# Kernel tuning notes

Hardware: AMD Instinct MI355X
Metric: run time of the kernel (lower is better)

## Reference

```python
import jax, jax.numpy as jnp
import numpy as np

B, S, E = 4, 2048, 1024
H = 16
D = E // H  # head dim = 64
ROPE_BASE = 10000.0


def _rope(t):
    # t: [B, H, S, D]; rotate-half RoPE (YaRN with scale=1 reduces to this)
    half = D // 2
    inv_freq = 1.0 / (ROPE_BASE ** (jnp.arange(0, half, dtype=jnp.float32) / half))
    pos = jnp.arange(t.shape[2], dtype=jnp.float32)
    ang = pos[:, None] * inv_freq[None, :]          # [S, D/2]
    cos, sin = jnp.cos(ang), jnp.sin(ang)
    t1, t2 = t[..., :half], t[..., half:]
    return jnp.concatenate([t1 * cos - t2 * sin, t1 * sin + t2 * cos], axis=-1)


def setup_inputs() -> dict:
    key = jax.random.key(0)
    ks = jax.random.split(key, 6)
    sc = 1.0 / np.sqrt(E)
    return {
        "x": jax.random.normal(ks[0], (B, S, E), jnp.float32),
        "Wq": jax.random.normal(ks[1], (E, E), jnp.float32) * sc,
        "Wk": jax.random.normal(ks[2], (E, E), jnp.float32) * sc,
        "Wv": jax.random.normal(ks[3], (E, E), jnp.float32) * sc,
        "Wp": jax.random.normal(ks[4], (E, E), jnp.float32) * sc,
        "bp": jnp.zeros((E,), jnp.float32),
    }


def reference(x, Wq, Wk, Wv, Wp, bp):
    seq = x.shape[1]
    def heads(W):
        # project then split heads -> [B, H, S, D]
        return (x @ W.T).reshape(B, seq, H, D).transpose(0, 2, 1, 3)
    q = _rope(heads(Wq))
    k = _rope(heads(Wk))
    v = heads(Wv)
    score = jnp.einsum("bhqd,bhkd->bhqk", q, k) * (D ** -0.5)
    mask = jnp.tril(jnp.ones((seq, seq), dtype=bool))
    score = jnp.where(mask[None, None], score, -jnp.inf)
    attn = jax.nn.softmax(score, axis=-1)
    out = jnp.einsum("bhqk,bhkd->bhqd", attn, v)
    out = out.transpose(0, 2, 1, 3).reshape(B, seq, E)
    return out @ Wp.T + bp  # dropout is identity at inference
```

## Files before the change

### kernel.cpp

```cpp
#include <hip/hip_runtime.h>
#include <hip/hip_bf16.h>

typedef __hip_bfloat16 bf16;
typedef __attribute__((ext_vector_type(8))) short bf16x8;
typedef __attribute__((ext_vector_type(4))) short bf16x4;
typedef __attribute__((ext_vector_type(4))) float f32x4;

static constexpr int B_ = 4, S_ = 2048, E_ = 1024, H_ = 16, D_ = 64;
static constexpr int M_ = B_ * S_;
static constexpr int NQKV = 3 * E_;

__device__ __forceinline__ void gload_lds16(const void* g, void* l) {
  __builtin_amdgcn_global_load_lds(
      (const __attribute__((address_space(1))) unsigned int*)g,
      (__attribute__((address_space(3))) unsigned int*)l, 16, 0, 0);
}

__device__ __forceinline__ void cast8(const float* __restrict__ src,
                                      bf16* __restrict__ dst, int t) {
  float4 a = ((const float4*)src)[2 * t];
  float4 b = ((const float4*)src)[2 * t + 1];
  union { bf16x8 v; bf16 e[8]; } u;
  u.e[0] = __float2bfloat16(a.x); u.e[1] = __float2bfloat16(a.y);
  u.e[2] = __float2bfloat16(a.z); u.e[3] = __float2bfloat16(a.w);
  u.e[4] = __float2bfloat16(b.x); u.e[5] = __float2bfloat16(b.y);
  u.e[6] = __float2bfloat16(b.z); u.e[7] = __float2bfloat16(b.w);
  ((bf16x8*)dst)[t] = u.v;
}

__global__ void prep_kernel(const float* __restrict__ x, const float* __restrict__ Wq,
                            const float* __restrict__ Wk, const float* __restrict__ Wv,
                            const float* __restrict__ Wp,
                            bf16* __restrict__ x_bf, bf16* __restrict__ w_bf,
                            float2* __restrict__ qtab, float2* __restrict__ ktab) {
  int bid = blockIdx.x;
  if (bid < 4096) {
    cast8(x, x_bf, bid * 256 + threadIdx.x);
  } else if (bid < 6144) {
    int wi = (bid - 4096) >> 9;
    const float* src = wi == 0 ? Wq : wi == 1 ? Wk : wi == 2 ? Wv : Wp;
    cast8(src, w_bf + (size_t)wi * E_ * E_, ((bid - 4096) & 511) * 256 + threadIdx.x);
  } else {
    int tt = (bid - 6144) * 256 + threadIdx.x;
    int i = tt & 31, s = tt >> 5;
    float inv_freq = powf(10000.0f, -(float)i / 32.0f);
    float ang = (float)s * inv_freq;
    float c = cosf(ang), sn = sinf(ang);
    const float qsc = 0.18033688011112043f;
    qtab[tt] = make_float2(c * qsc, sn * qsc);
    ktab[tt] = make_float2(c, sn);
  }
}

template <int OUTMODE>
__launch_bounds__(256)
__global__ void gemm_bt_kernel(const bf16* __restrict__ A, int lda,
                               const bf16* __restrict__ Bw, int ldb,
                               void* __restrict__ Cv, int ldc,
                               const float* __restrict__ bias,
                               int K, int ntiles_n,
                               const float2* __restrict__ qtab,
                               const float2* __restrict__ ktab,
                               bf16* __restrict__ qh,
                               bf16* __restrict__ khsw,
                               bf16* __restrict__ vtsw) {
  __shared__ bf16 Asm[128 * 64];
  __shared__ bf16 Bsm[128 * 64];
  int t = threadIdx.x;
  int lane = t & 63, w = t >> 6;
  int wr = w >> 1, wc = w & 1;
  int l15 = lane & 15, l4 = lane >> 4;
  int n0 = (blockIdx.x % ntiles_n) * 128;
  int m0 = (blockIdx.x / ntiles_n) * 128;

  f32x4 acc[4][4];
#pragma unroll
  for (int i = 0; i < 4; i++)
#pragma unroll
    for (int j = 0; j < 4; j++) acc[i][j] = (f32x4){0.f, 0.f, 0.f, 0.f};

  for (int k0 = 0; k0 < K; k0 += 64) {
#pragma unroll
    for (int p = 0; p < 4; p++) {
      int c = p * 256 + t;
      int row = c >> 3, kg = c & 7;
      int kgs = kg ^ (row & 7);
      const bf16* ga = A + (size_t)(m0 + row) * lda + k0 + kgs * 8;
      gload_lds16(ga, &Asm[(p * 256 + w * 64) * 8]);
      const bf16* gb = Bw + (size_t)(n0 + row) * ldb + k0 + kgs * 8;
      gload_lds16(gb, &Bsm[(p * 256 + w * 64) * 8]);
    }
    __syncthreads();
#pragma unroll
    for (int kk = 0; kk < 2; kk++) {
      bf16x8 am[4], bn[4];
#pragma unroll
      for (int i = 0; i < 4; i++) {
        int ra = wr * 64 + i * 16 + l15;
        am[i] = *(const bf16x8*)&Asm[ra * 64 + ((kk * 32 + l4 * 8) ^ ((ra & 7) * 8))];
        int rb = wc * 64 + i * 16 + l15;
        bn[i] = *(const bf16x8*)&Bsm[rb * 64 + ((kk * 32 + l4 * 8) ^ ((rb & 7) * 8))];
      }
#pragma unroll
      for (int i = 0; i < 4; i++)
#pragma unroll
        for (int j = 0; j < 4; j++)
          acc[i][j] = __builtin_amdgcn_mfma_f32_16x16x32_bf16(am[i], bn[j], acc[i][j], 0, 0, 0);
    }
    __syncthreads();
  }

  if (OUTMODE == 1) {
#pragma unroll
    for (int i = 0; i < 4; i++)
#pragma unroll
      for (int j = 0; j < 4; j++)
#pragma unroll
        for (int r = 0; r < 4; r++) {
          int m = m0 + wr * 64 + i * 16 + l4 * 4 + r;
          int n = n0 + wc * 64 + j * 16 + l15;
          ((float*)Cv)[(size_t)m * ldc + n] = acc[i][j][r] + bias[n];
        }
  } else {
    int btype = n0 >> 10;
    int h = ((n0 & 1023) >> 6) + wc;
    if (btype < 2) {
      const float2* tab = (btype == 0) ? qtab : ktab;
#pragma unroll
      for (int i = 0; i < 4; i++) {
        int mbase = m0 + wr * 64 + i * 16 + l4 * 4;
#pragma unroll
        for (int r = 0; r < 4; r++) {
          int m = mbase + r;
          int s = m & 2047, b = m >> 11;
#pragma unroll
          for (int j = 0; j < 2; j++) {
            int d1 = j * 16 + l15;
            float2 cs = tab[s * 32 + d1];
            float t1 = acc[i][j][r], t2 = acc[i][j + 2][r];
            bf16 o1 = __float2bfloat16(t1 * cs.x - t2 * cs.y);
            bf16 o2 = __float2bfloat16(t1 * cs.y + t2 * cs.x);
            if (btype == 0) {
              bf16* dst = qh + ((size_t)(b * H_ + h) * S_ + s) * D_;
              dst[d1] = o1;
              dst[d1 + 32] = o2;
            } else {
              int row = s & 63, kt = s >> 6, sz = (row & 7) * 8;
              bf16* dst = khsw + (((size_t)(b * H_ + h) * 32 + kt) * 64 + row) * 64;
              dst[d1 ^ sz] = o1;
              dst[(d1 + 32) ^ sz] = o2;
            }
          }
        }
      }
    } else {
#pragma unroll
      for (int i = 0; i < 4; i++) {
        int mbase = m0 + wr * 64 + i * 16 + l4 * 4;
        int c0 = mbase & 63, kt = (mbase >> 6) & 31, b = mbase >> 11;
#pragma unroll
        for (int j = 0; j < 4; j++) {
          int d = j * 16 + l15;
          union { bf16x4 v; short e[4]; } pk;
#pragma unroll
          for (int r = 0; r < 4; r++) {
            bf16 tv = __float2bfloat16(acc[i][j][r]);
            pk.e[r] = *(short*)&tv;
          }
          *(bf16x4*)&vtsw[(((size_t)(b * H_ + h) * 32 + kt) * 64 + d) * 64 +
                          (c0 ^ ((d & 7) * 8))] = pk.v;
        }
      }
    }
  }
}

__launch_bounds__(256, 3)
__global__ void attn_kernel(const bf16* __restrict__ qh, const bf16* __restrict__ khsw,
                            const bf16* __restrict__ vtsw, bf16* __restrict__ attn) {
  __shared__ bf16 Ksm[2][4096];
  __shared__ bf16 Vsm[2][4096];
  __shared__ bf16 Plds[4][2][16][72];
  int t = threadIdx.x, lane = t & 63, w = t >> 6;
  int l15 = lane & 15, l4 = lane >> 4;
  int swz = (l15 & 7) * 8;
  int st = 15 - (blockIdx.x >> 6);
  int bh = blockIdx.x & 63;
  int b = bh >> 4, h = bh & 15;
  const bf16* Qh = qh + (size_t)bh * S_ * D_;

#define STAGE(bb, kt)                                                          \
  do {                                                                         \
    const bf16* kb_ = khsw + ((size_t)bh * 32 + (kt)) * 4096 + w * 1024 + lane * 8; \
    const bf16* vb_ = vtsw + ((size_t)bh * 32 + (kt)) * 4096 + w * 1024 + lane * 8; \
    gload_lds16(kb_, &Ksm[bb][w * 1024]);                                      \
    gload_lds16(kb_ + 512, &Ksm[bb][w * 1024 + 512]);                          \
    gload_lds16(vb_, &Vsm[bb][w * 1024]);                                      \
    gload_lds16(vb_ + 512, &Vsm[bb][w * 1024 + 512]);                          \
  } while (0)

  int q0 = st * 128 + w * 32;
  int nt = 2 * st + 2;

  bf16x8 qf[2][2];
#pragma unroll
  for (int qg = 0; qg < 2; qg++)
#pragma unroll
    for (int sl = 0; sl < 2; sl++)
      qf[qg][sl] = *(const bf16x8*)&Qh[(size_t)(q0 + qg * 16 + l15) * D_ + sl * 32 + l4 * 8];

  f32x4 acc_o[2][4];
  float lsum[2] = {0.f, 0.f};
#pragma unroll
  for (int qg = 0; qg < 2; qg++)
#pragma unroll
    for (int j = 0; j < 4; j++) acc_o[qg][j] = (f32x4){0.f, 0.f, 0.f, 0.f};

  STAGE(0, 0);
  __syncthreads();
  int buf = 0;
  for (int ti = 0; ti < nt; ti++) {
    int kb = ti * 64;
    if (ti + 1 < nt) STAGE(buf ^ 1, ti + 1);
    if (kb <= q0 + 31) {
      bool maskt = (kb + 63 > q0);
      f32x4 s[2][4];
      __builtin_amdgcn_s_setprio(1);
#pragma unroll
      for (int cb = 0; cb < 4; cb++) {
        bf16x8 kf0 = *(const bf16x8*)&Ksm[buf][(cb * 16 + l15) * 64 + ((l4 * 8) ^ swz)];
        bf16x8 kf1 = *(const bf16x8*)&Ksm[buf][(cb * 16 + l15) * 64 + ((32 + l4 * 8) ^ swz)];
#pragma unroll
        for (int qg = 0; qg < 2; qg++) {
          f32x4 z = (f32x4){0.f, 0.f, 0.f, 0.f};
          z = __builtin_amdgcn_mfma_f32_16x16x32_bf16(kf0, qf[qg][0], z, 0, 0, 0);
          z = __builtin_amdgcn_mfma_f32_16x16x32_bf16(kf1, qf[qg][1], z, 0, 0, 0);
          s[qg][cb] = z;
        }
      }
      __builtin_amdgcn_s_setprio(0);
#pragma unroll
      for (int qg = 0; qg < 2; qg++) {
        int q = q0 + qg * 16 + l15;
#pragma unroll
        for (int cb = 0; cb < 4; cb++) {
          union { bf16x4 v; short e[4]; } pk;
#pragma unroll
          for (int r = 0; r < 4; r++) {
            float p = exp2f(s[qg][cb][r]);
            if (maskt && (kb + cb * 16 + l4 * 4 + r > q)) p = 0.f;
            lsum[qg] += p;
            bf16 pb16 = __float2bfloat16(p);
            pk.e[r] = *(short*)&pb16;
          }
          *(bf16x4*)&Plds[w][qg][l15][cb * 16 + l4 * 4] = pk.v;
        }
      }
      __builtin_amdgcn_s_setprio(1);
#pragma unroll
      for (int qg = 0; qg < 2; qg++) {
        bf16x8 pf0 = *(const bf16x8*)&Plds[w][qg][l15][l4 * 8];
        bf16x8 pf1 = *(const bf16x8*)&Plds[w][qg][l15][32 + l4 * 8];
#pragma unroll
        for (int db = 0; db < 4; db++) {
          bf16x8 vf0 = *(const bf16x8*)&Vsm[buf][(db * 16 + l15) * 64 + ((l4 * 8) ^ swz)];
          bf16x8 vf1 = *(const bf16x8*)&Vsm[buf][(db * 16 + l15) * 64 + ((32 + l4 * 8) ^ swz)];
          acc_o[qg][db] = __builtin_amdgcn_mfma_f32_16x16x32_bf16(pf0, vf0, acc_o[qg][db], 0, 0, 0);
          acc_o[qg][db] = __builtin_amdgcn_mfma_f32_16x16x32_bf16(pf1, vf1, acc_o[qg][db], 0, 0, 0);
        }
      }
      __builtin_amdgcn_s_setprio(0);
    }
    __syncthreads();
    buf ^= 1;
  }

  float invr[2][4];
#pragma unroll
  for (int qg = 0; qg < 2; qg++) {
    float ls = lsum[qg];
    ls += __shfl_xor(ls, 16, 64);
    ls += __shfl_xor(ls, 32, 64);
    float inv = 1.0f / ls;
#pragma unroll
    for (int r = 0; r < 4; r++) invr[qg][r] = __shfl(inv, l4 * 4 + r, 64);
  }

#pragma unroll
  for (int qg = 0; qg < 2; qg++)
#pragma unroll
    for (int db = 0; db < 4; db++)
#pragma unroll
      for (int r = 0; r < 4; r++) {
        int qa = q0 + qg * 16 + l4 * 4 + r;
        attn[(size_t)(b * S_ + qa) * E_ + h * 64 + db * 16 + l15] =
            __float2bfloat16(acc_o[qg][db][r] * invr[qg][r]);
      }
#undef STAGE
}

extern "C" void kernel_launch(void* const* d_in, const int* in_sizes, int n_in,
                              void* d_out, int out_size, void* d_ws, size_t ws_size,
                              hipStream_t stream) {
  const float* x  = (const float*)d_in[0];
  const float* Wq = (const float*)d_in[1];
  const float* Wk = (const float*)d_in[2];
  const float* Wv = (const float*)d_in[3];
  const float* Wp = (const float*)d_in[4];
  const float* bp = (const float*)d_in[5];

  char* ws = (char*)d_ws;
  bf16* x_bf   = (bf16*)(ws + 0);
  bf16* w_bf   = (bf16*)(ws + (16u << 20));
  bf16* aout   = (bf16*)(ws + (24u << 20));
  bf16* qh     = (bf16*)(ws + (40u << 20));
  bf16* khsw   = (bf16*)(ws + (56u << 20));
  bf16* vtsw   = (bf16*)(ws + (72u << 20));
  float2* qtab = (float2*)(ws + (88u << 20));
  float2* ktab = (float2*)(ws + (88u << 20) + (512u << 10));

  prep_kernel<<<6400, 256, 0, stream>>>(x, Wq, Wk, Wv, Wp, x_bf, w_bf, qtab, ktab);

  gemm_bt_kernel<2><<<(M_ / 128) * (NQKV / 128), 256, 0, stream>>>(
      x_bf, E_, w_bf, E_, nullptr, 0, nullptr, E_, NQKV / 128,
      qtab, ktab, qh, khsw, vtsw);

  attn_kernel<<<16 * 64, 256, 0, stream>>>(qh, khsw, vtsw, aout);

  gemm_bt_kernel<1><<<(M_ / 128) * (E_ / 128), 256, 0, stream>>>(
      aout, E_, w_bf + 3 * (size_t)E_ * E_, E_, d_out, E_, bp, E_, E_ / 128,
      nullptr, nullptr, nullptr, nullptr, nullptr);
}
```

Before: 176.4 us.

## Triple-buffer GEMM LDS stages with 256x128 tiles and 512-thread blocks

Reworks the projection GEMM into a three-stage LDS ring with global_load_lds prefetch two tiles ahead. It uses manual vmcnt waits and a single barrier per iteration instead of two syncthreads. The block tile grows to 256x128 with 8 waves, so B tiles are reused across more rows, and MFMA issue gets raised priority via setprio. LDS use rises to about 144KB per block, which limits occupancy, and the grid shrinks by half.

```diff
diff --git a/kernel.cpp b/kernel.cpp
--- a/kernel.cpp
+++ b/kernel.cpp
@@ -53,7 +53,7 @@
 }
 
 template <int OUTMODE>
-__launch_bounds__(256)
+__launch_bounds__(512, 2)
 __global__ void gemm_bt_kernel(const bf16* __restrict__ A, int lda,
                                const bf16* __restrict__ Bw, int ldb,
                                void* __restrict__ Cv, int ldc,
@@ -64,14 +64,29 @@
                                bf16* __restrict__ qh,
                                bf16* __restrict__ khsw,
                                bf16* __restrict__ vtsw) {
-  __shared__ bf16 Asm[128 * 64];
-  __shared__ bf16 Bsm[128 * 64];
+  __shared__ bf16 Asm[3][256 * 64];
+  __shared__ bf16 Bsm[3][128 * 64];
   int t = threadIdx.x;
-  int lane = t & 63, w = t >> 6;
-  int wr = w >> 1, wc = w & 1;
+  int lane = t & 63, wid = t >> 6;
+  int wm = wid >> 1, wn = wid & 1;
   int l15 = lane & 15, l4 = lane >> 4;
   int n0 = (blockIdx.x % ntiles_n) * 128;
-  int m0 = (blockIdx.x / ntiles_n) * 128;
+  int m0 = (blockIdx.x / ntiles_n) * 256;
+
+  int trow = t >> 3;
+  int tkg = ((t & 7) ^ (trow & 7)) * 8;
+  const bf16* Abase = A + (size_t)(m0 + trow) * lda + tkg;
+  const bf16* Bbase = Bw + (size_t)(n0 + trow) * ldb + tkg;
+
+#define GSTAGE(sb, kt)                                                         \
+  do {                                                                         \
+    const bf16* as_ = Abase + (size_t)(kt) * 64;                               \
+    _Pragma("unroll") for (int p = 0; p < 4; p++)                              \
+        gload_lds16(as_ + (size_t)p * 64 * lda, &Asm[sb][(p * 512 + t) * 8]);  \
+    const bf16* bs_ = Bbase + (size_t)(kt) * 64;                               \
+    _Pragma("unroll") for (int p = 0; p < 2; p++)                              \
+        gload_lds16(bs_ + (size_t)p * 64 * ldb, &Bsm[sb][(p * 512 + t) * 8]);  \
+  } while (0)
 
   f32x4 acc[4][4];
 #pragma unroll
@@ -79,36 +94,48 @@
 #pragma unroll
     for (int j = 0; j < 4; j++) acc[i][j] = (f32x4){0.f, 0.f, 0.f, 0.f};
 
-  for (int k0 = 0; k0 < K; k0 += 64) {
-#pragma unroll
-    for (int p = 0; p < 4; p++) {
-      int c = p * 256 + t;
-      int row = c >> 3, kg = c & 7;
-      int kgs = kg ^ (row & 7);
-      const bf16* ga = A + (size_t)(m0 + row) * lda + k0 + kgs * 8;
-      gload_lds16(ga, &Asm[(p * 256 + w * 64) * 8]);
-      const bf16* gb = Bw + (size_t)(n0 + row) * ldb + k0 + kgs * 8;
-      gload_lds16(gb, &Bsm[(p * 256 + w * 64) * 8]);
+  int NT = K >> 6;
+  GSTAGE(0, 0);
+  GSTAGE(1, 1);
+  asm volatile("s_waitcnt vmcnt(6)" ::: "memory");
+  __builtin_amdgcn_s_barrier();
+
+  int cur = 0;
+  for (int ti = 0; ti < NT; ti++) {
+    int sb = cur + 2; if (sb >= 3) sb -= 3;
+    bool more = (ti + 2 < NT);
+    if (more) GSTAGE(sb, ti + 2);
+
+    bf16x8 am[4][2], bn[4][2];
+#pragma unroll
+    for (int i = 0; i < 4; i++) {
+      int ra = wm * 64 + i * 16 + l15;
+      int rsw = (ra & 7) * 8;
+      am[i][0] = *(const bf16x8*)&Asm[cur][ra * 64 + ((l4 * 8) ^ rsw)];
+      am[i][1] = *(const bf16x8*)&Asm[cur][ra * 64 + ((32 + l4 * 8) ^ rsw)];
+      int rb = wn * 64 + i * 16 + l15;
+      bn[i][0] = *(const bf16x8*)&Bsm[cur][rb * 64 + ((l4 * 8) ^ rsw)];
+      bn[i][1] = *(const bf16x8*)&Bsm[cur][rb * 64 + ((32 + l4 * 8) ^ rsw)];
     }
-    __syncthreads();
-#pragma unroll
-    for (int kk = 0; kk < 2; kk++) {
-      bf16x8 am[4], bn[4];
-#pragma unroll
-      for (int i = 0; i < 4; i++) {
-        int ra = wr * 64 + i * 16 + l15;
-        am[i] = *(const bf16x8*)&Asm[ra * 64 + ((kk * 32 + l4 * 8) ^ ((ra & 7) * 8))];
-        int rb = wc * 64 + i * 16 + l15;
-        bn[i] = *(const bf16x8*)&Bsm[rb * 64 + ((kk * 32 + l4 * 8) ^ ((rb & 7) * 8))];
-      }
+    __builtin_amdgcn_s_setprio(1);
+#pragma unroll
+    for (int kk = 0; kk < 2; kk++)
 #pragma unroll
       for (int i = 0; i < 4; i++)
 #pragma unroll
         for (int j = 0; j < 4; j++)
-          acc[i][j] = __builtin_amdgcn_mfma_f32_16x16x32_bf16(am[i], bn[j], acc[i][j], 0, 0, 0);
+          acc[i][j] = __builtin_amdgcn_mfma_f32_16x16x32_bf16(am[i][kk], bn[j][kk], acc[i][j], 0, 0, 0);
+    __builtin_amdgcn_s_setprio(0);
+
+    if (more) {
+      asm volatile("s_waitcnt vmcnt(6)" ::: "memory");
+    } else {
+      asm volatile("s_waitcnt vmcnt(0)" ::: "memory");
     }
-    __syncthreads();
-  }
+    __builtin_amdgcn_s_barrier();
+    cur = cur + 1; if (cur >= 3) cur -= 3;
+  }
+#undef GSTAGE
 
   if (OUTMODE == 1) {
 #pragma unroll
@@ -117,18 +144,18 @@
       for (int j = 0; j < 4; j++)
 #pragma unroll
         for (int r = 0; r < 4; r++) {
-          int m = m0 + wr * 64 + i * 16 + l4 * 4 + r;
-          int n = n0 + wc * 64 + j * 16 + l15;
+          int m = m0 + wm * 64 + i * 16 + l4 * 4 + r;
+          int n = n0 + wn * 64 + j * 16 + l15;
           ((float*)Cv)[(size_t)m * ldc + n] = acc[i][j][r] + bias[n];
         }
   } else {
     int btype = n0 >> 10;
-    int h = ((n0 & 1023) >> 6) + wc;
+    int h = ((n0 & 1023) >> 6) + wn;
     if (btype < 2) {
       const float2* tab = (btype == 0) ? qtab : ktab;
 #pragma unroll
       for (int i = 0; i < 4; i++) {
-        int mbase = m0 + wr * 64 + i * 16 + l4 * 4;
+        int mbase = m0 + wm * 64 + i * 16 + l4 * 4;
 #pragma unroll
         for (int r = 0; r < 4; r++) {
           int m = mbase + r;
@@ -156,7 +183,7 @@
     } else {
 #pragma unroll
       for (int i = 0; i < 4; i++) {
-        int mbase = m0 + wr * 64 + i * 16 + l4 * 4;
+        int mbase = m0 + wm * 64 + i * 16 + l4 * 4;
         int c0 = mbase & 63, kt = (mbase >> 6) & 31, b = mbase >> 11;
 #pragma unroll
         for (int j = 0; j < 4; j++) {
@@ -321,13 +348,13 @@
 
   prep_kernel<<<6400, 256, 0, stream>>>(x, Wq, Wk, Wv, Wp, x_bf, w_bf, qtab, ktab);
 
-  gemm_bt_kernel<2><<<(M_ / 128) * (NQKV / 128), 256, 0, stream>>>(
+  gemm_bt_kernel<2><<<(M_ / 256) * (NQKV / 128), 512, 0, stream>>>(
       x_bf, E_, w_bf, E_, nullptr, 0, nullptr, E_, NQKV / 128,
       qtab, ktab, qh, khsw, vtsw);
 
   attn_kernel<<<16 * 64, 256, 0, stream>>>(qh, khsw, vtsw, aout);
 
-  gemm_bt_kernel<1><<<(M_ / 128) * (E_ / 128), 256, 0, stream>>>(
+  gemm_bt_kernel<1><<<(M_ / 256) * (E_ / 128), 512, 0, stream>>>(
       aout, E_, w_bf + 3 * (size_t)E_ * E_, E_, d_out, E_, bp, E_, E_ / 128,
       nullptr, nullptr, nullptr, nullptr, nullptr);
 }
```

Measured after the change: 200.9 us. 13.9% more time.

## Rewrite GEMM as 256x256 tile, 8-wave, double-buffered ping-pong pipeline

Applied to the files above, without the earlier changes.

Both projection GEMMs move from 128x128 tiles with 4 waves and a single LDS buffer to 256x256 tiles with 8 waves. The K loop is double-buffered and split into quadrant phases, so global-to-LDS loads overlap MFMA work. The schedule uses explicit barriers, waitcnt and setprio, and block indices are swizzled across XCDs for cache locality. The aim is to hide load latency and raise data reuse per tile. In exchange the kernel uses 128KB of LDS and more registers, and the grid is much smaller (384 and 128 blocks), which may leave CUs idle.

```diff
diff --git a/kernel.cpp b/kernel.cpp
--- a/kernel.cpp
+++ b/kernel.cpp
@@ -53,7 +53,7 @@
 }
 
 template <int OUTMODE>
-__launch_bounds__(256)
+__launch_bounds__(512, 2)
 __global__ void gemm_bt_kernel(const bf16* __restrict__ A, int lda,
                                const bf16* __restrict__ Bw, int ldb,
                                void* __restrict__ Cv, int ldc,
@@ -64,71 +64,161 @@
                                bf16* __restrict__ qh,
                                bf16* __restrict__ khsw,
                                bf16* __restrict__ vtsw) {
-  __shared__ bf16 Asm[128 * 64];
-  __shared__ bf16 Bsm[128 * 64];
+  __shared__ bf16 Asm[2][256 * 64];
+  __shared__ bf16 Bsm[2][256 * 64];
   int t = threadIdx.x;
-  int lane = t & 63, w = t >> 6;
-  int wr = w >> 1, wc = w & 1;
+  int lane = t & 63, wid = t >> 6;
+  int wm = wid >> 2, wn = wid & 3;
   int l15 = lane & 15, l4 = lane >> 4;
-  int n0 = (blockIdx.x % ntiles_n) * 128;
-  int m0 = (blockIdx.x / ntiles_n) * 128;
-
-  f32x4 acc[4][4];
-#pragma unroll
-  for (int i = 0; i < 4; i++)
+  int l8 = lane >> 3, c8 = lane & 7;
+  int csw = (c8 ^ l8) * 8;
+
+  int cpx = gridDim.x >> 3;
+  int swb = (blockIdx.x & 7) * cpx + (blockIdx.x >> 3);
+  int n0 = (swb % ntiles_n) * 256;
+  int m0 = (swb / ntiles_n) * 256;
+
+#define STAGE_A(sb, kt, mh)                                                    \
+  do {                                                                         \
+    _Pragma("unroll") for (int i_ = 0; i_ < 2; i_++) {                         \
+      int lrb = i_ * 128 + (mh) * 64 + wid * 8;                                \
+      gload_lds16(A + (size_t)(m0 + lrb + l8) * lda + (kt) * 64 + csw,         \
+                  &Asm[sb][lrb * 64]);                                         \
+    }                                                                          \
+  } while (0)
+
+#define STAGE_B(sb, kt, nh)                                                    \
+  do {                                                                         \
+    _Pragma("unroll") for (int i_ = 0; i_ < 2; i_++) {                         \
+      int hb = i_ * 64 + wid * 8;                                              \
+      int nrb = (hb >> 5) * 64 + (nh) * 32 + (hb & 31);                        \
+      gload_lds16(Bw + (size_t)(n0 + nrb + l8) * ldb + (kt) * 64 + csw,        \
+                  &Bsm[sb][nrb * 64]);                                         \
+    }                                                                          \
+  } while (0)
+
+#define LDA(cbuf, mh)                                                          \
+  do {                                                                         \
+    _Pragma("unroll") for (int i_ = 0; i_ < 4; i_++) {                         \
+      int ra = wm * 128 + (mh) * 64 + i_ * 16 + l15;                           \
+      int rs = (ra & 7) * 8;                                                   \
+      am[i_][0] = *(const bf16x8*)&Asm[cbuf][ra * 64 + ((l4 * 8) ^ rs)];       \
+      am[i_][1] = *(const bf16x8*)&Asm[cbuf][ra * 64 + ((32 + l4 * 8) ^ rs)];  \
+    }                                                                          \
+  } while (0)
+
+#define LDB(cbuf, nh)                                                          \
+  do {                                                                         \
+    _Pragma("unroll") for (int j_ = 0; j_ < 2; j_++) {                         \
+      int rb = wn * 64 + (nh) * 32 + j_ * 16 + l15;                            \
+      int rs = (rb & 7) * 8;                                                   \
+      bn[nh][j_][0] = *(const bf16x8*)&Bsm[cbuf][rb * 64 + ((l4 * 8) ^ rs)];   \
+      bn[nh][j_][1] = *(const bf16x8*)&Bsm[cbuf][rb * 64 + ((32 + l4 * 8) ^ rs)]; \
+    }                                                                          \
+  } while (0)
+
+#define QUAD(mh, nh)                                                           \
+  do {                                                                         \
+    __builtin_amdgcn_s_setprio(1);                                             \
+    _Pragma("unroll") for (int kk_ = 0; kk_ < 2; kk_++)                        \
+      _Pragma("unroll") for (int i_ = 0; i_ < 4; i_++)                         \
+        _Pragma("unroll") for (int j_ = 0; j_ < 2; j_++)                       \
+          acc[(mh) * 4 + i_][(nh) * 2 + j_] =                                  \
+              __builtin_amdgcn_mfma_f32_16x16x32_bf16(                         \
+                  am[i_][kk_], bn[nh][j_][kk_],                                \
+                  acc[(mh) * 4 + i_][(nh) * 2 + j_], 0, 0, 0);                 \
+    __builtin_amdgcn_s_setprio(0);                                             \
+  } while (0)
+
+#define PH_SYNC_R                                                              \
+  __builtin_amdgcn_s_barrier();                                                \
+  asm volatile("s_waitcnt lgkmcnt(0)" ::: "memory");                           \
+  __builtin_amdgcn_sched_barrier(0)
+
+  f32x4 acc[8][4];
+#pragma unroll
+  for (int i = 0; i < 8; i++)
 #pragma unroll
     for (int j = 0; j < 4; j++) acc[i][j] = (f32x4){0.f, 0.f, 0.f, 0.f};
-
-  for (int k0 = 0; k0 < K; k0 += 64) {
-#pragma unroll
-    for (int p = 0; p < 4; p++) {
-      int c = p * 256 + t;
-      int row = c >> 3, kg = c & 7;
-      int kgs = kg ^ (row & 7);
-      const bf16* ga = A + (size_t)(m0 + row) * lda + k0 + kgs * 8;
-      gload_lds16(ga, &Asm[(p * 256 + w * 64) * 8]);
-      const bf16* gb = Bw + (size_t)(n0 + row) * ldb + k0 + kgs * 8;
-      gload_lds16(gb, &Bsm[(p * 256 + w * 64) * 8]);
-    }
-    __syncthreads();
-#pragma unroll
-    for (int kk = 0; kk < 2; kk++) {
-      bf16x8 am[4], bn[4];
-#pragma unroll
-      for (int i = 0; i < 4; i++) {
-        int ra = wr * 64 + i * 16 + l15;
-        am[i] = *(const bf16x8*)&Asm[ra * 64 + ((kk * 32 + l4 * 8) ^ ((ra & 7) * 8))];
-        int rb = wc * 64 + i * 16 + l15;
-        bn[i] = *(const bf16x8*)&Bsm[rb * 64 + ((kk * 32 + l4 * 8) ^ ((rb & 7) * 8))];
-      }
-#pragma unroll
-      for (int i = 0; i < 4; i++)
-#pragma unroll
-        for (int j = 0; j < 4; j++)
-          acc[i][j] = __builtin_amdgcn_mfma_f32_16x16x32_bf16(am[i], bn[j], acc[i][j], 0, 0, 0);
-    }
-    __syncthreads();
+  bf16x8 am[4][2];
+  bf16x8 bn[2][2][2];
+
+  int NI = K >> 7;
+  STAGE_A(0, 0, 0); STAGE_A(0, 0, 1); STAGE_B(0, 0, 0); STAGE_B(0, 0, 1);
+  STAGE_A(1, 1, 0); STAGE_A(1, 1, 1);
+  asm volatile("s_waitcnt vmcnt(4)" ::: "memory");
+  __builtin_amdgcn_s_barrier();
+
+  for (int it = 0; it < NI; it++) {
+    int T = 2 * it;
+    bool more = (it + 1 < NI);
+    LDA(0, 0); LDB(0, 0);
+    STAGE_B(1, T + 1, 0); STAGE_B(1, T + 1, 1);
+    PH_SYNC_R;
+    QUAD(0, 0);
+    __builtin_amdgcn_s_barrier();
+    LDB(0, 1);
+    if (more) STAGE_A(0, T + 2, 0);
+    PH_SYNC_R;
+    QUAD(0, 1);
+    __builtin_amdgcn_s_barrier();
+    LDA(0, 1);
+    PH_SYNC_R;
+    QUAD(1, 0);
+    __builtin_amdgcn_s_barrier();
+    if (more) STAGE_A(0, T + 2, 1);
+    __builtin_amdgcn_s_barrier();
+    QUAD(1, 1);
+    if (more) asm volatile("s_waitcnt vmcnt(4)" ::: "memory");
+    else      asm volatile("s_waitcnt vmcnt(0)" ::: "memory");
+    __builtin_amdgcn_s_barrier();
+    LDA(1, 0); LDB(1, 0);
+    if (more) STAGE_B(0, T + 2, 0);
+    PH_SYNC_R;
+    QUAD(0, 0);
+    __builtin_amdgcn_s_barrier();
+    LDB(1, 1);
+    if (more) STAGE_B(0, T + 2, 1);
+    PH_SYNC_R;
+    QUAD(0, 1);
+    __builtin_amdgcn_s_barrier();
+    LDA(1, 1);
+    if (more) STAGE_A(1, T + 3, 0);
+    PH_SYNC_R;
+    QUAD(1, 0);
+    __builtin_amdgcn_s_barrier();
+    if (more) STAGE_A(1, T + 3, 1);
+    __builtin_amdgcn_s_barrier();
+    QUAD(1, 1);
+    if (more) asm volatile("s_waitcnt vmcnt(4)" ::: "memory");
+    __builtin_amdgcn_s_barrier();
   }
+#undef STAGE_A
+#undef STAGE_B
+#undef LDA
+#undef LDB
+#undef QUAD
+#undef PH_SYNC_R
 
   if (OUTMODE == 1) {
 #pragma unroll
-    for (int i = 0; i < 4; i++)
+    for (int mi = 0; mi < 8; mi++)
 #pragma unroll
       for (int j = 0; j < 4; j++)
 #pragma unroll
         for (int r = 0; r < 4; r++) {
-          int m = m0 + wr * 64 + i * 16 + l4 * 4 + r;
-          int n = n0 + wc * 64 + j * 16 + l15;
-          ((float*)Cv)[(size_t)m * ldc + n] = acc[i][j][r] + bias[n];
+          int m = m0 + wm * 128 + mi * 16 + l4 * 4 + r;
+          int n = n0 + wn * 64 + j * 16 + l15;
+          ((float*)Cv)[(size_t)m * ldc + n] = acc[mi][j][r] + bias[n];
         }
   } else {
     int btype = n0 >> 10;
-    int h = ((n0 & 1023) >> 6) + wc;
+    int h = ((n0 & 1023) >> 6) + wn;
     if (btype < 2) {
       const float2* tab = (btype == 0) ? qtab : ktab;
 #pragma unroll
-      for (int i = 0; i < 4; i++) {
-        int mbase = m0 + wr * 64 + i * 16 + l4 * 4;
+      for (int mi = 0; mi < 8; mi++) {
+        int mbase = m0 + wm * 128 + mi * 16 + l4 * 4;
 #pragma unroll
         for (int r = 0; r < 4; r++) {
           int m = mbase + r;
@@ -137,7 +227,7 @@
           for (int j = 0; j < 2; j++) {
             int d1 = j * 16 + l15;
             float2 cs = tab[s * 32 + d1];
-            float t1 = acc[i][j][r], t2 = acc[i][j + 2][r];
+            float t1 = acc[mi][j][r], t2 = acc[mi][j + 2][r];
             bf16 o1 = __float2bfloat16(t1 * cs.x - t2 * cs.y);
             bf16 o2 = __float2bfloat16(t1 * cs.y + t2 * cs.x);
             if (btype == 0) {
@@ -155,8 +245,8 @@
       }
     } else {
 #pragma unroll
-      for (int i = 0; i < 4; i++) {
-        int mbase = m0 + wr * 64 + i * 16 + l4 * 4;
+      for (int mi = 0; mi < 8; mi++) {
+        int mbase = m0 + wm * 128 + mi * 16 + l4 * 4;
         int c0 = mbase & 63, kt = (mbase >> 6) & 31, b = mbase >> 11;
 #pragma unroll
         for (int j = 0; j < 4; j++) {
@@ -164,7 +254,7 @@
           union { bf16x4 v; short e[4]; } pk;
 #pragma unroll
           for (int r = 0; r < 4; r++) {
-            bf16 tv = __float2bfloat16(acc[i][j][r]);
+            bf16 tv = __float2bfloat16(acc[mi][j][r]);
             pk.e[r] = *(short*)&tv;
           }
           *(bf16x4*)&vtsw[(((size_t)(b * H_ + h) * 32 + kt) * 64 + d) * 64 +
@@ -321,13 +411,13 @@
 
   prep_kernel<<<6400, 256, 0, stream>>>(x, Wq, Wk, Wv, Wp, x_bf, w_bf, qtab, ktab);
 
-  gemm_bt_kernel<2><<<(M_ / 128) * (NQKV / 128), 256, 0, stream>>>(
-      x_bf, E_, w_bf, E_, nullptr, 0, nullptr, E_, NQKV / 128,
+  gemm_bt_kernel<2><<<(M_ / 256) * (NQKV / 256), 512, 0, stream>>>(
+      x_bf, E_, w_bf, E_, nullptr, 0, nullptr, E_, NQKV / 256,
       qtab, ktab, qh, khsw, vtsw);
 
   attn_kernel<<<16 * 64, 256, 0, stream>>>(qh, khsw, vtsw, aout);
 
-  gemm_bt_kernel<1><<<(M_ / 128) * (E_ / 128), 256, 0, stream>>>(
-      aout, E_, w_bf + 3 * (size_t)E_ * E_, E_, d_out, E_, bp, E_, E_ / 128,
+  gemm_bt_kernel<1><<<(M_ / 256) * (E_ / 256), 512, 0, stream>>>(
+      aout, E_, w_bf + 3 * (size_t)E_ * E_, E_, d_out, E_, bp, E_, E_ / 256,
       nullptr, nullptr, nullptr, nullptr, nullptr);
 }
```

New measurement: 211.8 us. 1.2x slower.

## Double-buffer LDS tiles in GEMM to overlap global loads with MFMA

Applied to the files above, without the earlier changes.

The GEMM main loop now uses two LDS buffers for the A and B tiles, issuing global-to-LDS loads for the next K tile before computing on the current one. Per-thread base addresses are precomputed once, and one barrier per iteration is removed. The goal is to hide global memory latency behind the matrix instructions. The cost is twice the LDS use (64KB per block), which can lower occupancy.

```diff
diff --git a/kernel.cpp b/kernel.cpp
--- a/kernel.cpp
+++ b/kernel.cpp
@@ -64,8 +64,8 @@
                                bf16* __restrict__ qh,
                                bf16* __restrict__ khsw,
                                bf16* __restrict__ vtsw) {
-  __shared__ bf16 Asm[128 * 64];
-  __shared__ bf16 Bsm[128 * 64];
+  __shared__ bf16 Asm[2][128 * 64];
+  __shared__ bf16 Bsm[2][128 * 64];
   int t = threadIdx.x;
   int lane = t & 63, w = t >> 6;
   int wr = w >> 1, wc = w & 1;
@@ -73,33 +73,42 @@
   int n0 = (blockIdx.x % ntiles_n) * 128;
   int m0 = (blockIdx.x / ntiles_n) * 128;
 
+  int trow = t >> 3;
+  int tkg = ((t & 7) ^ (trow & 7)) * 8;
+  const bf16* Abase = A + (size_t)(m0 + trow) * lda + tkg;
+  const bf16* Bbase = Bw + (size_t)(n0 + trow) * ldb + tkg;
+
+#define GSTAGE(sb, kt)                                                         \
+  do {                                                                         \
+    const bf16* as_ = Abase + (size_t)(kt) * 64;                               \
+    const bf16* bs_ = Bbase + (size_t)(kt) * 64;                               \
+    _Pragma("unroll") for (int p = 0; p < 4; p++) {                            \
+      gload_lds16(as_ + (size_t)p * 32 * lda, &Asm[sb][(p * 256 + t) * 8]);    \
+      gload_lds16(bs_ + (size_t)p * 32 * ldb, &Bsm[sb][(p * 256 + t) * 8]);    \
+    }                                                                          \
+  } while (0)
+
   f32x4 acc[4][4];
 #pragma unroll
   for (int i = 0; i < 4; i++)
 #pragma unroll
     for (int j = 0; j < 4; j++) acc[i][j] = (f32x4){0.f, 0.f, 0.f, 0.f};
 
-  for (int k0 = 0; k0 < K; k0 += 64) {
-#pragma unroll
-    for (int p = 0; p < 4; p++) {
-      int c = p * 256 + t;
-      int row = c >> 3, kg = c & 7;
-      int kgs = kg ^ (row & 7);
-      const bf16* ga = A + (size_t)(m0 + row) * lda + k0 + kgs * 8;
-      gload_lds16(ga, &Asm[(p * 256 + w * 64) * 8]);
-      const bf16* gb = Bw + (size_t)(n0 + row) * ldb + k0 + kgs * 8;
-      gload_lds16(gb, &Bsm[(p * 256 + w * 64) * 8]);
-    }
-    __syncthreads();
+  int NT = K >> 6;
+  GSTAGE(0, 0);
+  __syncthreads();
+  int buf = 0;
+  for (int ti = 0; ti < NT; ti++) {
+    if (ti + 1 < NT) GSTAGE(buf ^ 1, ti + 1);
 #pragma unroll
     for (int kk = 0; kk < 2; kk++) {
       bf16x8 am[4], bn[4];
 #pragma unroll
       for (int i = 0; i < 4; i++) {
         int ra = wr * 64 + i * 16 + l15;
-        am[i] = *(const bf16x8*)&Asm[ra * 64 + ((kk * 32 + l4 * 8) ^ ((ra & 7) * 8))];
+        am[i] = *(const bf16x8*)&Asm[buf][ra * 64 + ((kk * 32 + l4 * 8) ^ ((ra & 7) * 8))];
         int rb = wc * 64 + i * 16 + l15;
-        bn[i] = *(const bf16x8*)&Bsm[rb * 64 + ((kk * 32 + l4 * 8) ^ ((rb & 7) * 8))];
+        bn[i] = *(const bf16x8*)&Bsm[buf][rb * 64 + ((kk * 32 + l4 * 8) ^ ((rb & 7) * 8))];
       }
 #pragma unroll
       for (int i = 0; i < 4; i++)
@@ -108,7 +117,9 @@
           acc[i][j] = __builtin_amdgcn_mfma_f32_16x16x32_bf16(am[i], bn[j], acc[i][j], 0, 0, 0);
     }
     __syncthreads();
-  }
+    buf ^= 1;
+  }
+#undef GSTAGE
 
   if (OUTMODE == 1) {
 #pragma unroll
```

Measured after the change: 188.7 us. +7.0%, slower.
